# Performance work log

Measured on AMD Instinct MI355X. Metric: run time of the kernel, lower is better.

The kernel has to match this reference:

```python
import jax, jax.numpy as jnp
import numpy as np

B, N, C, H, P, DP = 2, 512, 384, 12, 4, 128
CH = C // H
SCALE = CH ** -0.5
EPS = 1e-5


def setup_inputs() -> dict:
    key = jax.random.key(0)
    ks = jax.random.split(key, 16)
    w = lambda k, i, o: jax.random.normal(k, (i, o), jnp.float32) * 0.02
    inp = {
        'single': jax.random.normal(ks[0], (B, N, C), jnp.float32),
        'pair': jax.random.normal(ks[1], (B, N, N, DP), jnp.float32),
        'rot': jax.random.normal(ks[2], (B, N, 3, 3), jnp.float32),
        'trans': jax.random.normal(ks[3], (B, N, 3), jnp.float32),
        'mask': jnp.ones((B, N), jnp.float32),
        'Wq': w(ks[4], C, C), 'bq': jnp.zeros((C,)),
        'Wk': w(ks[5], C, C), 'bk': jnp.zeros((C,)),
        'Wv': w(ks[6], C, C), 'bv': jnp.zeros((C,)),
        'Wpb': w(ks[7], DP, H), 'bpb': jnp.zeros((H,)),
        'Wqp': w(ks[8], C, H * P * 3), 'bqp': jnp.zeros((H * P * 3,)),
        'Wkp': w(ks[9], C, H * P * 3), 'bkp': jnp.zeros((H * P * 3,)),
        'Wvp': w(ks[10], C, H * P * 3), 'bvp': jnp.zeros((H * P * 3,)),
        'Wo': w(ks[11], C, C), 'bo': jnp.zeros((C,)),
        'Wpo': w(ks[12], H * P * 3, C), 'bpo': jnp.zeros((C,)),
        'ln_g': jnp.ones((C,)), 'ln_b': jnp.zeros((C,)),
    }
    return inp


def _to_global(pts, rot, trans):
    # pts: [B,N,H,P,3], rot: [B,N,3,3], trans: [B,N,3]
    return jnp.einsum('bnhpd,bnde->bnhpe', pts, rot) + trans[:, :, None, None, :]


def reference(single, pair, rot, trans, mask,
              Wq, bq, Wk, bk, Wv, bv, Wpb, bpb,
              Wqp, bqp, Wkp, bkp, Wvp, bvp,
              Wo, bo, Wpo, bpo, ln_g, ln_b):
    q = (single @ Wq + bq).reshape(B, N, H, CH)
    k = (single @ Wk + bk).reshape(B, N, H, CH)
    v = (single @ Wv + bv).reshape(B, N, H, CH)
    pair_bias = jnp.transpose(pair @ Wpb + bpb, (0, 3, 1, 2))  # [B,H,N,N]

    q_pts = (single @ Wqp + bqp).reshape(B, N, H, P, 3)
    k_pts = (single @ Wkp + bkp).reshape(B, N, H, P, 3)
    qg = _to_global(q_pts, rot, trans)
    kg = _to_global(k_pts, rot, trans)

    q2 = jnp.sum(qg * qg, axis=(3, 4))  # [B,N,H]
    k2 = jnp.sum(kg * kg, axis=(3, 4))
    qk = jnp.einsum('bnhpd,bmhpd->bhnm', qg, kg)
    q2h = jnp.transpose(q2, (0, 2, 1))  # [B,H,N]
    k2h = jnp.transpose(k2, (0, 2, 1))
    point_logits = -0.5 * (q2h[..., :, None] + k2h[..., None, :] - 2.0 * qk) * SCALE

    scalar_logits = jnp.einsum('bnhc,bmhc->bhnm', q, k) * SCALE
    logits = scalar_logits + pair_bias + point_logits

    mask2d = mask[:, None, :, None] * mask[:, None, None, :]  # [B,1,N,N]
    logits = jnp.where(mask2d == 0, -1e9, logits)
    attn = jax.nn.softmax(logits, axis=-1)

    weighted_scalar = jnp.einsum('bhnm,bmhc->bnhc', attn, v).reshape(B, N, C)

    v_pts = (single @ Wvp + bvp).reshape(B, N, H, P, 3)
    vg = _to_global(v_pts, rot, trans)
    weighted_points = jnp.einsum('bhnm,bmhpd->bnhpd', attn, vg).reshape(B, N, H * P * 3)

    point_proj = weighted_points @ Wpo + bpo
    out = (weighted_scalar + point_proj) @ Wo + bo

    x = single + out
    mu = jnp.mean(x, axis=-1, keepdims=True)
    var = jnp.mean((x - mu) ** 2, axis=-1, keepdims=True)
    return (x - mu) * jax.lax.rsqrt(var + EPS) * ln_g + ln_b
```

## Files before the change

### kernel.cpp

```cpp
#include <hip/hip_runtime.h>
#include <hip/hip_bf16.h>

#define Bb   2
#define Nn   512
#define Cc   384
#define Hh   12
#define BN   1024
#define NC1  1584
#define CT1  99
#define SCALE 0.17677669529663687f

typedef __attribute__((ext_vector_type(8))) short short8;
typedef __attribute__((ext_vector_type(4))) float f32x4;

__device__ __forceinline__ unsigned short f2bf(float f){
  union { float f; unsigned u; } v; v.f = f;
  unsigned u = v.u;
  unsigned r = u + 0x7fffu + ((u >> 16) & 1u);
  return (unsigned short)(r >> 16);
}
__device__ __forceinline__ float bf_lo(unsigned u){ union{unsigned u; float f;} v; v.u = u << 16; return v.f; }
__device__ __forceinline__ float bf_hi(unsigned u){ union{unsigned u; float f;} v; v.u = u & 0xffff0000u; return v.f; }
__device__ __forceinline__ unsigned pack2(float a, float b){
  return (unsigned)f2bf(a) | ((unsigned)f2bf(b) << 16);
}

__device__ __forceinline__ void bias_job(const float* __restrict__ pair,
    const float* __restrict__ Wpb, const float* __restrict__ bpb,
    unsigned short* __restrict__ biasf, int jid, int tid)
{
  int l = tid & 63, w = tid >> 6;
  long m0 = (long)jid * 64 + w * 16;
  long m = m0 + (l & 15);
  int kb = (l >> 4) << 3;
  int col = l & 15;
  short8 bf[4];
#pragma unroll
  for (int t = 0; t < 4; ++t){
#pragma unroll
    for (int j = 0; j < 8; ++j){
      int k = t * 32 + kb + j;
      float v = (col < 12) ? Wpb[k * 12 + col] : 0.f;
      bf[t][j] = (short)f2bf(v);
    }
  }
  const float* pr = pair + m * 128 + kb;
  f32x4 acc = {0,0,0,0};
#pragma unroll
  for (int t = 0; t < 4; ++t){
    float4 x0 = *(const float4*)(pr + t * 32);
    float4 x1 = *(const float4*)(pr + t * 32 + 4);
    short8 a;
    a[0] = (short)f2bf(x0.x); a[1] = (short)f2bf(x0.y);
    a[2] = (short)f2bf(x0.z); a[3] = (short)f2bf(x0.w);
    a[4] = (short)f2bf(x1.x); a[5] = (short)f2bf(x1.y);
    a[6] = (short)f2bf(x1.z); a[7] = (short)f2bf(x1.w);
    acc = __builtin_amdgcn_mfma_f32_16x16x32_bf16(a, bf[t], acc, 0, 0, 0);
  }
  int h = col;
  if (h < 12){
    long mr = m0 + ((l >> 4) << 2);
    int b  = (int)(mr >> 18);
    int i  = (int)((mr >> 9) & 511);
    int j  = (int)(mr & 511);
    int jt = j >> 5, f = (j >> 4) & 1, g2 = (j >> 2) & 3;
    int qt = i >> 4, q = i & 15;
    float bb = bpb[h];
    long e16 = (((((long)((b * 12 + h) * 16 + jt) * 32 + qt) * 2 + f) * 64) + (g2 * 16 + q)) * 4;
    uint2 wv; wv.x = pack2(acc[0] + bb, acc[1] + bb); wv.y = pack2(acc[2] + bb, acc[3] + bb);
    *(uint2*)(biasf + e16) = wv;
  }
}

__global__ __launch_bounds__(256) void k1_prep_bias(
    const float* __restrict__ single,
    const float* __restrict__ Wq, const float* __restrict__ Wk, const float* __restrict__ Wv,
    const float* __restrict__ Wqp, const float* __restrict__ Wkp, const float* __restrict__ Wvp,
    const float* __restrict__ bq, const float* __restrict__ bk, const float* __restrict__ bv,
    const float* __restrict__ bqp, const float* __restrict__ bkp, const float* __restrict__ bvp,
    const float* __restrict__ Wpo, const float* __restrict__ Wo,
    const float* __restrict__ pair, const float* __restrict__ Wpb, const float* __restrict__ bpb,
    unsigned short* __restrict__ sbf, unsigned short* __restrict__ wcat, float* __restrict__ bcat,
    unsigned short* __restrict__ wpof, unsigned short* __restrict__ wof,
    unsigned short* __restrict__ wppad, unsigned short* __restrict__ biasf)
{
  int bid = blockIdx.x, tid = threadIdx.x;
  if (bid >= 256){ bias_job(pair, Wpb, bpb, biasf, bid - 256, tid); return; }

  const int n0 = BN * Cc;
  const int n1 = 12 * CT1 * 512;
  const int n4 = NC1;
  const int n5 = 61440;
  const int n6 = 147456;
  const int n7 = BN * 16;
  const int total = n0 + n1 + n4 + n5 + n6 + n7;
  for (int i = bid * 256 + tid; i < total; i += 256 * 256){
    int e = i;
    if (e < n0){ sbf[e] = f2bf(single[e]); continue; }
    e -= n0;
    if (e < n1){
      int j8 = e & 7, l = (e >> 3) & 63, ctt = e >> 9;
      int ct = ctt % CT1, t = ctt / CT1;
      int k = t * 32 + ((l >> 4) << 3) + j8;
      int col = (ct << 4) + (l & 15);
      float v;
      if (col < 1152){
        const float* W = (col < 384) ? Wq : (col < 768 ? Wk : Wv);
        v = W[k * 384 + (col % 384)];
      } else {
        int c2 = col - 1152;
        const float* W = (c2 < 144) ? Wqp : (c2 < 288 ? Wkp : Wvp);
        v = W[k * 144 + (c2 % 144)];
      }
      wcat[e] = f2bf(v); continue;
    }
    e -= n1;
    if (e < n4){
      int col = e; float v;
      if (col < 1152){
        const float* bb = (col < 384) ? bq : (col < 768 ? bk : bv);
        v = bb[col % 384];
      } else {
        int c2 = col - 1152;
        const float* bb = (c2 < 144) ? bqp : (c2 < 288 ? bkp : bvp);
        v = bb[c2 % 144];
      }
      bcat[col] = v; continue;
    }
    e -= n4;
    if (e < n5){
      int j8 = e & 7, l = (e >> 3) & 63, ctt = e >> 9;
      int ct = ctt % 24, t = ctt / 24;
      int k = t * 32 + ((l >> 4) << 3) + j8;
      int col = (ct << 4) + (l & 15);
      wpof[e] = (k < 144) ? f2bf(Wpo[k * 384 + col]) : (unsigned short)0;
      continue;
    }
    e -= n5;
    if (e < n6){
      int j8 = e & 7, l = (e >> 3) & 63, ctt = e >> 9;
      int ct = ctt % 24, t = ctt / 24;
      int k = t * 32 + ((l >> 4) << 3) + j8;
      int col = (ct << 4) + (l & 15);
      wof[e] = f2bf(Wo[k * 384 + col]);
      continue;
    }
    e -= n6;
    { int row = e >> 4, c = e & 15; wppad[row * 160 + 144 + c] = 0; }
  }
}

__global__ __launch_bounds__(256) void k2_proj_bias(
    const unsigned short* __restrict__ sbf, const unsigned short* __restrict__ wcat,
    const float* __restrict__ bcat, float* __restrict__ proj,
    const float* __restrict__ pair, const float* __restrict__ Wpb, const float* __restrict__ bpb,
    unsigned short* __restrict__ biasf)
{
  int bid = blockIdx.x, tid = threadIdx.x;
  if (bid >= 528){ bias_job(pair, Wpb, bpb, biasf, 1024 + (bid - 528), tid); return; }

  int l = tid & 63, w = tid >> 6;
  int bx = bid & 15, by = bid >> 4;
  int m0 = bx * 64 + w * 16;
  const unsigned short* Ap = sbf + (long)(m0 + (l & 15)) * Cc + ((l >> 4) << 3);
  int ct0 = by * 3;
  f32x4 acc0 = {0,0,0,0}, acc1 = {0,0,0,0}, acc2 = {0,0,0,0};
  for (int t = 0; t < 12; ++t){
    short8 a = *(const short8*)(Ap + t * 32);
    const unsigned short* wp_ = wcat + ((long)(t * CT1 + ct0) * 64 + l) * 8;
    short8 b0 = *(const short8*)(wp_);
    short8 b1 = *(const short8*)(wp_ + 512);
    short8 b2 = *(const short8*)(wp_ + 1024);
    acc0 = __builtin_amdgcn_mfma_f32_16x16x32_bf16(a, b0, acc0, 0, 0, 0);
    acc1 = __builtin_amdgcn_mfma_f32_16x16x32_bf16(a, b1, acc1, 0, 0, 0);
    acc2 = __builtin_amdgcn_mfma_f32_16x16x32_bf16(a, b2, acc2, 0, 0, 0);
  }
  int rbase = m0 + ((l >> 4) << 2);
  int cb = by * 48 + (l & 15);
#pragma unroll
  for (int c = 0; c < 3; ++c){
    f32x4 ac = (c == 0) ? acc0 : (c == 1 ? acc1 : acc2);
    int col = cb + c * 16;
    float bb = bcat[col];
#pragma unroll
    for (int r = 0; r < 4; ++r)
      proj[(long)(rbase + r) * NC1 + col] = ac[r] + bb;
  }
}

__global__ __launch_bounds__(256) void k3_pack_bias(
    const float* __restrict__ proj, const float* __restrict__ rot,
    const float* __restrict__ trans, const float* __restrict__ mask,
    unsigned short* __restrict__ qf, unsigned short* __restrict__ kf,
    unsigned short* __restrict__ vf, float* __restrict__ q2h, float* __restrict__ k2h,
    const float* __restrict__ pair, const float* __restrict__ Wpb, const float* __restrict__ bpb,
    unsigned short* __restrict__ biasf)
{
  __shared__ float smemf[5792];
  int bid = blockIdx.x, tid = threadIdx.x;
  if (bid >= 384){ bias_job(pair, Wpb, bpb, biasf, 4096 + (bid - 384), tid); return; }

  float* scal = smemf;
  float* praw = scal + 3072;
  float* pg   = praw + 1152;
  float* rots = pg + 1152;
  float* trs  = rots + 288;
  float* msk  = trs + 96;

  int jid = bid;
  int b = jid / 192, rem = jid % 192;
  int h = rem >> 4, rt = rem & 15;
  int j0 = rt * 32;
  int bn0 = b * 512 + j0;
  int bh = b * 12 + h;

  for (int idx = tid; idx < 3072; idx += 256){
    int a = idx >> 10, row = (idx >> 5) & 31, c = idx & 31;
    scal[idx] = proj[(long)(bn0 + row) * NC1 + a * 384 + h * 32 + c];
  }
  for (int idx = tid; idx < 1152; idx += 256){
    int a = idx / 384, rr = idx % 384, row = rr / 12, pe = rr % 12;
    praw[idx] = proj[(long)(bn0 + row) * NC1 + 1152 + a * 144 + h * 12 + pe];
  }
  for (int idx = tid; idx < 288; idx += 256) rots[idx] = rot[(long)bn0 * 9 + idx];
  for (int idx = tid; idx < 96; idx += 256)  trs[idx] = trans[(long)bn0 * 3 + idx];
  for (int idx = tid; idx < 32; idx += 256)  msk[idx] = mask[bn0 + idx];
  __syncthreads();

  for (int idx = tid; idx < 1152; idx += 256){
    int a = idx / 384, rr = idx % 384, row = rr / 12, pe = rr % 12;
    int p = pe / 3, ee = pe % 3;
    pg[idx] = praw[a * 384 + row * 12 + p * 3] * rots[row * 9 + ee]
            + praw[a * 384 + row * 12 + p * 3 + 1] * rots[row * 9 + 3 + ee]
            + praw[a * 384 + row * 12 + p * 3 + 2] * rots[row * 9 + 6 + ee] + trs[row * 3 + ee];
  }
  __syncthreads();

  for (int idx = tid; idx < 64; idx += 256){
    int a = idx >> 5, row = idx & 31;
    float s2 = 0.f;
#pragma unroll
    for (int pe = 0; pe < 12; ++pe){ float g = pg[a * 384 + row * 12 + pe]; s2 += g * g; }
    float mv = msk[row];
    float rres = -0.5f * SCALE * s2 + (mv != 0.f ? 0.f : -2e9f);
    (a ? k2h : q2h)[(long)bh * 512 + j0 + row] = rres;
  }

  for (int idx = tid; idx < 2048; idx += 256){
    int a = idx >> 10, r = idx & 1023;
    int jjp = r & 3, l = (r >> 2) & 63, ks = (r >> 8) & 1, sub = r >> 9;
    int row = sub * 16 + (l & 15);
    int kk = ks * 32 + ((l >> 4) << 3) + jjp * 2;
    int k1 = kk + 1;
    float v0 = (kk < 32) ? scal[a * 1024 + row * 32 + kk] : (kk < 44 ? pg[a * 384 + row * 12 + kk - 32] : 0.f);
    float v1 = (k1 < 32) ? scal[a * 1024 + row * 32 + k1] : (k1 < 44 ? pg[a * 384 + row * 12 + k1 - 32] : 0.f);
    if (a == 0){ v0 *= SCALE; v1 *= SCALE; }
    unsigned* dst = (unsigned*)(a ? kf : qf);
    dst[((((long)bh * 32 + rt * 2 + sub) * 2 + ks) * 64 + l) * 4 + jjp] = pack2(v0, v1);
  }

  for (int idx = tid; idx < 768; idx += 256){
    int jjp = idx & 3, l = (idx >> 2) & 63, cf = idx >> 8;
    int c = cf * 16 + (l & 15);
    int j = ((l >> 4) << 3) + jjp * 2;
    float v0 = (c < 32) ? scal[2048 + j * 32 + c]       : (c < 44 ? pg[768 + j * 12 + (c - 32)]       : 0.f);
    float v1 = (c < 32) ? scal[2048 + (j + 1) * 32 + c] : (c < 44 ? pg[768 + (j + 1) * 12 + (c - 32)] : 0.f);
    ((unsigned*)vf)[(((long)bh * 16 + rt) * 3 + cf) * 256 + l * 4 + jjp] = pack2(v0, v1);
  }
}

__global__ __launch_bounds__(256) void attn2_kernel(
    const unsigned short* __restrict__ qf, const unsigned short* __restrict__ kf,
    const unsigned short* __restrict__ vf, const unsigned short* __restrict__ biasf,
    const float* __restrict__ q2h, const float* __restrict__ k2h,
    float* __restrict__ wsout, unsigned short* __restrict__ wpout)
{
  __shared__ unsigned short pls[4][16][40];
  __shared__ float oW[4][3][64][4];
  __shared__ float mW[4][16], lsW[4][16];
  __shared__ float fW[4][16], linvS[16];

  int l = threadIdx.x & 63, w = threadIdx.x >> 6;
  int qt = blockIdx.x, h = blockIdx.y, b = blockIdx.z;
  int bh = b * 12 + h;
  int g = l >> 4, q_ = l & 15;

  const short8* qp = (const short8*)(qf + (((long)(bh * 32 + qt) * 2) * 64 + l) * 8);
  short8 qA = qp[0], qB = qp[64];
  float cq = q2h[(long)bh * 512 + qt * 16 + q_];

  float m = -1e30f, ls = 0.f;
  f32x4 o0 = {0,0,0,0}, o1 = {0,0,0,0}, o2 = {0,0,0,0};
  const f32x4 z4 = {0,0,0,0};

#pragma unroll
  for (int ji = 0; ji < 4; ++ji){
    int jt = w * 4 + ji;
    const short8* kp = (const short8*)(kf + (((long)(bh * 32 + jt * 2) * 2) * 64 + l) * 8);
    short8 k00 = kp[0], k01 = kp[64], k10 = kp[128], k11 = kp[192];
    f32x4 s0 = __builtin_amdgcn_mfma_f32_16x16x32_bf16(k00, qA, z4, 0, 0, 0);
    s0 = __builtin_amdgcn_mfma_f32_16x16x32_bf16(k01, qB, s0, 0, 0, 0);
    f32x4 s1 = __builtin_amdgcn_mfma_f32_16x16x32_bf16(k10, qA, z4, 0, 0, 0);
    s1 = __builtin_amdgcn_mfma_f32_16x16x32_bf16(k11, qB, s1, 0, 0, 0);

    const uint2* bp = (const uint2*)(biasf + ((((long)(bh * 16 + jt) * 32 + qt) * 2) * 64) * 4);
    uint2 bb0 = bp[l], bb1 = bp[64 + l];
    const float4* k2p = (const float4*)(k2h + (long)bh * 512 + jt * 32);
    float4 ck0 = k2p[g], ck1 = k2p[4 + g];

    s0[0] += bf_lo(bb0.x) + cq + ck0.x;
    s0[1] += bf_hi(bb0.x) + cq + ck0.y;
    s0[2] += bf_lo(bb0.y) + cq + ck0.z;
    s0[3] += bf_hi(bb0.y) + cq + ck0.w;
    s1[0] += bf_lo(bb1.x) + cq + ck1.x;
    s1[1] += bf_hi(bb1.x) + cq + ck1.y;
    s1[2] += bf_lo(bb1.y) + cq + ck1.z;
    s1[3] += bf_hi(bb1.y) + cq + ck1.w;

    float tm = fmaxf(fmaxf(fmaxf(s0[0], s0[1]), fmaxf(s0[2], s0[3])),
                     fmaxf(fmaxf(s1[0], s1[1]), fmaxf(s1[2], s1[3])));
    tm = fmaxf(tm, __shfl_xor(tm, 16));
    tm = fmaxf(tm, __shfl_xor(tm, 32));
    float mn = fmaxf(m, tm);
    float alpha = __expf(m - mn);
    f32x4 p0, p1;
    float ts = 0.f;
#pragma unroll
    for (int r = 0; r < 4; ++r){ p0[r] = __expf(s0[r] - mn); ts += p0[r]; }
#pragma unroll
    for (int r = 0; r < 4; ++r){ p1[r] = __expf(s1[r] - mn); ts += p1[r]; }
    ts += __shfl_xor(ts, 16);
    ts += __shfl_xor(ts, 32);
    ls = ls * alpha + ts; m = mn;

    f32x4 av;
#pragma unroll
    for (int r = 0; r < 4; ++r) av[r] = __shfl(alpha, g * 4 + r);
#pragma unroll
    for (int r = 0; r < 4; ++r){ o0[r] *= av[r]; o1[r] *= av[r]; o2[r] *= av[r]; }

    uint2 w0; w0.x = pack2(p0[0], p0[1]); w0.y = pack2(p0[2], p0[3]);
    uint2 w1; w1.x = pack2(p1[0], p1[1]); w1.y = pack2(p1[2], p1[3]);
    *(uint2*)&pls[w][q_][g * 4]      = w0;
    *(uint2*)&pls[w][q_][16 + g * 4] = w1;
    short8 pa = *(const short8*)&pls[w][q_][g * 8];

    const short8* vp = (const short8*)(vf + (((long)(bh * 16 + jt) * 3) * 64 + l) * 8);
    short8 v0 = vp[0], v1 = vp[64], v2 = vp[128];
    o0 = __builtin_amdgcn_mfma_f32_16x16x32_bf16(pa, v0, o0, 0, 0, 0);
    o1 = __builtin_amdgcn_mfma_f32_16x16x32_bf16(pa, v1, o1, 0, 0, 0);
    o2 = __builtin_amdgcn_mfma_f32_16x16x32_bf16(pa, v2, o2, 0, 0, 0);
  }

  if (g == 0){ mW[w][q_] = m; lsW[w][q_] = ls; }
  *(f32x4*)&oW[w][0][l][0] = o0;
  *(f32x4*)&oW[w][1][l][0] = o1;
  *(f32x4*)&oW[w][2][l][0] = o2;
  __syncthreads();

  if (w == 0){
    float M = fmaxf(fmaxf(mW[0][q_], mW[1][q_]), fmaxf(mW[2][q_], mW[3][q_]));
    float f = __expf(mW[g][q_] - M);
    fW[g][q_] = f;
    float lf = lsW[g][q_] * f;
    lf += __shfl_xor(lf, 16);
    lf += __shfl_xor(lf, 32);
    if (g == 0) linvS[q_] = 1.f / lf;
  }
  __syncthreads();

  if (w < 3){
    float fr[4][4], li[4];
#pragma unroll
    for (int r = 0; r < 4; ++r){
      int q = g * 4 + r;
      li[r] = linvS[q];
#pragma unroll
      for (int vw = 0; vw < 4; ++vw) fr[vw][r] = fW[vw][q];
    }
    f32x4 sum = {0,0,0,0};
#pragma unroll
    for (int vw = 0; vw < 4; ++vw){
      f32x4 ov = *(const f32x4*)&oW[vw][w][l][0];
#pragma unroll
      for (int r = 0; r < 4; ++r) sum[r] += ov[r] * fr[vw][r];
    }
#pragma unroll
    for (int r = 0; r < 4; ++r){
      long bn = (long)b * 512 + qt * 16 + g * 4 + r;
      float val = sum[r] * li[r];
      if (w == 0)      wsout[bn * 384 + h * 32 + q_] = val;
      else if (w == 1) wsout[bn * 384 + h * 32 + 16 + q_] = val;
      else if (q_ < 12) wpout[bn * 160 + h * 12 + q_] = f2bf(val);
    }
  }
}

__global__ __launch_bounds__(256) void tail_kernel(
    const unsigned short* __restrict__ wpbuf, const unsigned short* __restrict__ wpof,
    const float* __restrict__ bpo, const float* __restrict__ wso,
    const unsigned short* __restrict__ wof, const float* __restrict__ bo,
    const float* __restrict__ single, const float* __restrict__ ln_g,
    const float* __restrict__ ln_b, float* __restrict__ out)
{
  __shared__ unsigned short t1s[16][392];
  __shared__ float redS[4][16], redQ[4][16];
  int l = threadIdx.x & 63, w = threadIdx.x >> 6;
  int m0 = blockIdx.x * 16;
  int rb = (l >> 4) << 2;
  int arow = m0 + (l & 15);

  {
    short8 awp[5];
    const unsigned short* Ap = wpbuf + (long)arow * 160 + ((l >> 4) << 3);
#pragma unroll
    for (int t = 0; t < 5; ++t) awp[t] = *(const short8*)(Ap + t * 32);
#pragma unroll
    for (int c6 = 0; c6 < 6; ++c6){
      int ct = w * 6 + c6;
      f32x4 acc = {0,0,0,0};
#pragma unroll
      for (int t = 0; t < 5; ++t){
        short8 bfr = *(const short8*)(wpof + ((long)(t * 24 + ct) * 64 + l) * 8);
        acc = __builtin_amdgcn_mfma_f32_16x16x32_bf16(awp[t], bfr, acc, 0, 0, 0);
      }
      int col = ct * 16 + (l & 15);
      float bb = bpo[col];
#pragma unroll
      for (int r = 0; r < 4; ++r){
        float v = acc[r] + bb + wso[(long)(m0 + rb + r) * 384 + col];
        t1s[rb + r][col] = f2bf(v);
      }
    }
  }
  __syncthreads();

  short8 a2[12];
  {
    int lr = l & 15;
#pragma unroll
    for (int t = 0; t < 12; ++t)
      a2[t] = *(const short8*)&t1s[lr][t * 32 + ((l >> 4) << 3)];
  }
  f32x4 xa[6];
  float s1[4] = {0,0,0,0}, s2[4] = {0,0,0,0};
#pragma unroll
  for (int c6 = 0; c6 < 6; ++c6){
    int ct = w * 6 + c6;
    f32x4 acc = {0,0,0,0};
#pragma unroll
    for (int t = 0; t < 12; ++t){
      short8 bfr = *(const short8*)(wof + ((long)(t * 24 + ct) * 64 + l) * 8);
      acc = __builtin_amdgcn_mfma_f32_16x16x32_bf16(a2[t], bfr, acc, 0, 0, 0);
    }
    int col = ct * 16 + (l & 15);
    float bb = bo[col];
#pragma unroll
    for (int r = 0; r < 4; ++r){
      float v = acc[r] + bb + single[(long)(m0 + rb + r) * 384 + col];
      acc[r] = v; s1[r] += v; s2[r] += v * v;
    }
    xa[c6] = acc;
  }
#pragma unroll
  for (int off = 1; off < 16; off <<= 1){
#pragma unroll
    for (int r = 0; r < 4; ++r){
      s1[r] += __shfl_xor(s1[r], off);
      s2[r] += __shfl_xor(s2[r], off);
    }
  }
  if ((l & 15) == 0){
#pragma unroll
    for (int r = 0; r < 4; ++r){ redS[w][rb + r] = s1[r]; redQ[w][rb + r] = s2[r]; }
  }
  __syncthreads();
  float mu[4], inv[4];
#pragma unroll
  for (int r = 0; r < 4; ++r){
    float ts = redS[0][rb + r] + redS[1][rb + r] + redS[2][rb + r] + redS[3][rb + r];
    float tq = redQ[0][rb + r] + redQ[1][rb + r] + redQ[2][rb + r] + redQ[3][rb + r];
    mu[r] = ts * (1.f / 384.f);
    float var = tq * (1.f / 384.f) - mu[r] * mu[r];
    inv[r] = rsqrtf(var + 1e-5f);
  }
#pragma unroll
  for (int c6 = 0; c6 < 6; ++c6){
    int ct = w * 6 + c6;
    int col = ct * 16 + (l & 15);
    float g = ln_g[col], bt = ln_b[col];
#pragma unroll
    for (int r = 0; r < 4; ++r)
      out[(long)(m0 + rb + r) * 384 + col] = (xa[c6][r] - mu[r]) * inv[r] * g + bt;
  }
}

extern "C" void kernel_launch(void* const* d_in, const int* in_sizes, int n_in,
                              void* d_out, int out_size, void* d_ws, size_t ws_size,
                              hipStream_t stream)
{
  const float* single = (const float*)d_in[0];
  const float* pair   = (const float*)d_in[1];
  const float* rot    = (const float*)d_in[2];
  const float* trans  = (const float*)d_in[3];
  const float* mask   = (const float*)d_in[4];
  const float* Wq  = (const float*)d_in[5];  const float* bq  = (const float*)d_in[6];
  const float* Wk  = (const float*)d_in[7];  const float* bk  = (const float*)d_in[8];
  const float* Wv  = (const float*)d_in[9];  const float* bv  = (const float*)d_in[10];
  const float* Wpb = (const float*)d_in[11]; const float* bpb = (const float*)d_in[12];
  const float* Wqp = (const float*)d_in[13]; const float* bqp = (const float*)d_in[14];
  const float* Wkp = (const float*)d_in[15]; const float* bkp = (const float*)d_in[16];
  const float* Wvp = (const float*)d_in[17]; const float* bvp = (const float*)d_in[18];
  const float* Wo  = (const float*)d_in[19]; const float* bo  = (const float*)d_in[20];
  const float* Wpo = (const float*)d_in[21]; const float* bpo = (const float*)d_in[22];
  const float* ln_g = (const float*)d_in[23]; const float* ln_b = (const float*)d_in[24];

  char* wsb = (char*)d_ws;
  size_t off = 0;
  auto alloc = [&](size_t bytes) -> void* {
    void* p = wsb + off; off += (bytes + 255) & ~(size_t)255; return p;
  };
  unsigned short* sbf  = (unsigned short*)alloc((size_t)BN * Cc * 2);
  unsigned short* wcat = (unsigned short*)alloc((size_t)12 * CT1 * 512 * 2);
  unsigned short* wpof = (unsigned short*)alloc((size_t)5 * 24 * 512 * 2);
  unsigned short* wof  = (unsigned short*)alloc((size_t)12 * 24 * 512 * 2);
  float* bcat  = (float*)alloc(NC1 * 4);
  float* proj  = (float*)alloc((size_t)BN * NC1 * 4);
  unsigned short* biasf = (unsigned short*)alloc((size_t)Bb * Hh * Nn * Nn * 2);
  unsigned short* qfragb = (unsigned short*)alloc((size_t)786432 * 2);
  unsigned short* kfragb = (unsigned short*)alloc((size_t)786432 * 2);
  unsigned short* vfragb = (unsigned short*)alloc((size_t)589824 * 2);
  float* q2hb  = (float*)alloc((size_t)12288 * 4);
  float* k2hb  = (float*)alloc((size_t)12288 * 4);
  float* wso   = (float*)alloc((size_t)BN * 384 * 4);
  unsigned short* wpbuf = (unsigned short*)alloc((size_t)BN * 160 * 2);
  if (off > ws_size) return;

  k1_prep_bias<<<256 + 1024, 256, 0, stream>>>(
      single, Wq, Wk, Wv, Wqp, Wkp, Wvp, bq, bk, bv, bqp, bkp, bvp, Wpo, Wo,
      pair, Wpb, bpb, sbf, wcat, bcat, wpof, wof, wpbuf, biasf);
  k2_proj_bias<<<528 + 3072, 256, 0, stream>>>(
      sbf, wcat, bcat, proj, pair, Wpb, bpb, biasf);
  k3_pack_bias<<<384 + 4096, 256, 0, stream>>>(
      proj, rot, trans, mask, qfragb, kfragb, vfragb, q2hb, k2hb,
      pair, Wpb, bpb, biasf);
  attn2_kernel<<<dim3(32, 12, 2), 256, 0, stream>>>(qfragb, kfragb, vfragb, biasf,
                                                    q2hb, k2hb, wso, wpbuf);
  tail_kernel<<<64, 256, 0, stream>>>(wpbuf, wpof, bpo, wso, wof, bo,
                                      single, ln_g, ln_b, (float*)d_out);
}
```

Measured before the change: 106.2 us.

## Overlap pair-bias computation with per-batch attention and tail across fused kernels

Splits the attention kernel by batch so that batch 0 attention runs in the same launch as the last part of the pair-bias projection (batch 1), and batch 1 attention runs alongside the tail for batch 0. The bias work in k3 is halved and the remainder moves into k4, which lets the bias, attention and tail stages run concurrently instead of serially. This adds a kernel launch and depends on the bias job indices and batch boundaries being split correctly, so that batch 0's bias is complete before k4 and batch 1's bias is complete before k5.

```diff
diff --git a/kernel.cpp b/kernel.cpp
--- a/kernel.cpp
+++ b/kernel.cpp
@@ -69,6 +69,238 @@
     long e16 = (((((long)((b * 12 + h) * 16 + jt) * 32 + qt) * 2 + f) * 64) + (g2 * 16 + q)) * 4;
     uint2 wv; wv.x = pack2(acc[0] + bb, acc[1] + bb); wv.y = pack2(acc[2] + bb, acc[3] + bb);
     *(uint2*)(biasf + e16) = wv;
+  }
+}
+
+__device__ __forceinline__ void attn_job(
+    const unsigned short* __restrict__ qf, const unsigned short* __restrict__ kf,
+    const unsigned short* __restrict__ vf, const unsigned short* __restrict__ biasf,
+    const float* __restrict__ q2h, const float* __restrict__ k2h,
+    float* __restrict__ wsout, unsigned short* __restrict__ wpout,
+    int b, int jid, int tid, unsigned char* smem)
+{
+  unsigned short* pls = (unsigned short*)smem;
+  float* oW   = (float*)(smem + 5120);
+  float* mW   = (float*)(smem + 17408);
+  float* lsW  = (float*)(smem + 17664);
+  float* fW   = (float*)(smem + 17920);
+  float* linvS= (float*)(smem + 18176);
+
+  int l = tid & 63, w = tid >> 6;
+  int qt = jid & 31, h = jid >> 5;
+  int bh = b * 12 + h;
+  int g = l >> 4, q_ = l & 15;
+
+  const short8* qp = (const short8*)(qf + (((long)(bh * 32 + qt) * 2) * 64 + l) * 8);
+  short8 qA = qp[0], qB = qp[64];
+  float cq = q2h[(long)bh * 512 + qt * 16 + q_];
+
+  float m = -1e30f, ls = 0.f;
+  f32x4 o0 = {0,0,0,0}, o1 = {0,0,0,0}, o2 = {0,0,0,0};
+  const f32x4 z4 = {0,0,0,0};
+
+#pragma unroll
+  for (int ji = 0; ji < 4; ++ji){
+    int jt = w * 4 + ji;
+    const short8* kp = (const short8*)(kf + (((long)(bh * 32 + jt * 2) * 2) * 64 + l) * 8);
+    short8 k00 = kp[0], k01 = kp[64], k10 = kp[128], k11 = kp[192];
+    f32x4 s0 = __builtin_amdgcn_mfma_f32_16x16x32_bf16(k00, qA, z4, 0, 0, 0);
+    s0 = __builtin_amdgcn_mfma_f32_16x16x32_bf16(k01, qB, s0, 0, 0, 0);
+    f32x4 s1 = __builtin_amdgcn_mfma_f32_16x16x32_bf16(k10, qA, z4, 0, 0, 0);
+    s1 = __builtin_amdgcn_mfma_f32_16x16x32_bf16(k11, qB, s1, 0, 0, 0);
+
+    const uint2* bp = (const uint2*)(biasf + ((((long)(bh * 16 + jt) * 32 + qt) * 2) * 64) * 4);
+    uint2 bb0 = bp[l], bb1 = bp[64 + l];
+    const float4* k2p = (const float4*)(k2h + (long)bh * 512 + jt * 32);
+    float4 ck0 = k2p[g], ck1 = k2p[4 + g];
+
+    s0[0] += bf_lo(bb0.x) + cq + ck0.x;
+    s0[1] += bf_hi(bb0.x) + cq + ck0.y;
+    s0[2] += bf_lo(bb0.y) + cq + ck0.z;
+    s0[3] += bf_hi(bb0.y) + cq + ck0.w;
+    s1[0] += bf_lo(bb1.x) + cq + ck1.x;
+    s1[1] += bf_hi(bb1.x) + cq + ck1.y;
+    s1[2] += bf_lo(bb1.y) + cq + ck1.z;
+    s1[3] += bf_hi(bb1.y) + cq + ck1.w;
+
+    float tm = fmaxf(fmaxf(fmaxf(s0[0], s0[1]), fmaxf(s0[2], s0[3])),
+                     fmaxf(fmaxf(s1[0], s1[1]), fmaxf(s1[2], s1[3])));
+    tm = fmaxf(tm, __shfl_xor(tm, 16));
+    tm = fmaxf(tm, __shfl_xor(tm, 32));
+    float mn = fmaxf(m, tm);
+    float alpha = __expf(m - mn);
+    f32x4 p0, p1;
+    float ts = 0.f;
+#pragma unroll
+    for (int r = 0; r < 4; ++r){ p0[r] = __expf(s0[r] - mn); ts += p0[r]; }
+#pragma unroll
+    for (int r = 0; r < 4; ++r){ p1[r] = __expf(s1[r] - mn); ts += p1[r]; }
+    ts += __shfl_xor(ts, 16);
+    ts += __shfl_xor(ts, 32);
+    ls = ls * alpha + ts; m = mn;
+
+    f32x4 av;
+#pragma unroll
+    for (int r = 0; r < 4; ++r) av[r] = __shfl(alpha, g * 4 + r);
+#pragma unroll
+    for (int r = 0; r < 4; ++r){ o0[r] *= av[r]; o1[r] *= av[r]; o2[r] *= av[r]; }
+
+    uint2 w0; w0.x = pack2(p0[0], p0[1]); w0.y = pack2(p0[2], p0[3]);
+    uint2 w1; w1.x = pack2(p1[0], p1[1]); w1.y = pack2(p1[2], p1[3]);
+    *(uint2*)&pls[(w * 16 + q_) * 40 + g * 4]      = w0;
+    *(uint2*)&pls[(w * 16 + q_) * 40 + 16 + g * 4] = w1;
+    short8 pa = *(const short8*)&pls[(w * 16 + q_) * 40 + g * 8];
+
+    const short8* vp = (const short8*)(vf + (((long)(bh * 16 + jt) * 3) * 64 + l) * 8);
+    short8 v0 = vp[0], v1 = vp[64], v2 = vp[128];
+    o0 = __builtin_amdgcn_mfma_f32_16x16x32_bf16(pa, v0, o0, 0, 0, 0);
+    o1 = __builtin_amdgcn_mfma_f32_16x16x32_bf16(pa, v1, o1, 0, 0, 0);
+    o2 = __builtin_amdgcn_mfma_f32_16x16x32_bf16(pa, v2, o2, 0, 0, 0);
+  }
+
+  if (g == 0){ mW[w * 16 + q_] = m; lsW[w * 16 + q_] = ls; }
+  *(f32x4*)&oW[((w * 3 + 0) * 64 + l) * 4] = o0;
+  *(f32x4*)&oW[((w * 3 + 1) * 64 + l) * 4] = o1;
+  *(f32x4*)&oW[((w * 3 + 2) * 64 + l) * 4] = o2;
+  __syncthreads();
+
+  if (w == 0){
+    float M = fmaxf(fmaxf(mW[q_], mW[16 + q_]), fmaxf(mW[32 + q_], mW[48 + q_]));
+    float f = __expf(mW[g * 16 + q_] - M);
+    fW[g * 16 + q_] = f;
+    float lf = lsW[g * 16 + q_] * f;
+    lf += __shfl_xor(lf, 16);
+    lf += __shfl_xor(lf, 32);
+    if (g == 0) linvS[q_] = 1.f / lf;
+  }
+  __syncthreads();
+
+  if (w < 3){
+    float fr[4][4], li[4];
+#pragma unroll
+    for (int r = 0; r < 4; ++r){
+      int q = g * 4 + r;
+      li[r] = linvS[q];
+#pragma unroll
+      for (int vw = 0; vw < 4; ++vw) fr[vw][r] = fW[vw * 16 + q];
+    }
+    f32x4 sum = {0,0,0,0};
+#pragma unroll
+    for (int vw = 0; vw < 4; ++vw){
+      f32x4 ov = *(const f32x4*)&oW[((vw * 3 + w) * 64 + l) * 4];
+#pragma unroll
+      for (int r = 0; r < 4; ++r) sum[r] += ov[r] * fr[vw][r];
+    }
+#pragma unroll
+    for (int r = 0; r < 4; ++r){
+      long bn = (long)b * 512 + qt * 16 + g * 4 + r;
+      float val = sum[r] * li[r];
+      if (w == 0)      wsout[bn * 384 + h * 32 + q_] = val;
+      else if (w == 1) wsout[bn * 384 + h * 32 + 16 + q_] = val;
+      else if (q_ < 12) wpout[bn * 160 + h * 12 + q_] = f2bf(val);
+    }
+  }
+}
+
+__device__ __forceinline__ void tail_job(
+    const unsigned short* __restrict__ wpbuf, const unsigned short* __restrict__ wpof,
+    const float* __restrict__ bpo, const float* __restrict__ wso,
+    const unsigned short* __restrict__ wof, const float* __restrict__ bo,
+    const float* __restrict__ single, const float* __restrict__ ln_g,
+    const float* __restrict__ ln_b, float* __restrict__ out,
+    int jid, int tid, unsigned char* smem)
+{
+  unsigned short* t1s = (unsigned short*)smem;
+  float* redS = (float*)(smem + 12544);
+  float* redQ = (float*)(smem + 12800);
+
+  int l = tid & 63, w = tid >> 6;
+  int m0 = jid * 16;
+  int rb = (l >> 4) << 2;
+  int arow = m0 + (l & 15);
+
+  {
+    short8 awp[5];
+    const unsigned short* Ap = wpbuf + (long)arow * 160 + ((l >> 4) << 3);
+#pragma unroll
+    for (int t = 0; t < 5; ++t) awp[t] = *(const short8*)(Ap + t * 32);
+#pragma unroll
+    for (int c6 = 0; c6 < 6; ++c6){
+      int ct = w * 6 + c6;
+      f32x4 acc = {0,0,0,0};
+#pragma unroll
+      for (int t = 0; t < 5; ++t){
+        short8 bfr = *(const short8*)(wpof + ((long)(t * 24 + ct) * 64 + l) * 8);
+        acc = __builtin_amdgcn_mfma_f32_16x16x32_bf16(awp[t], bfr, acc, 0, 0, 0);
+      }
+      int col = ct * 16 + (l & 15);
+      float bb = bpo[col];
+#pragma unroll
+      for (int r = 0; r < 4; ++r){
+        float v = acc[r] + bb + wso[(long)(m0 + rb + r) * 384 + col];
+        t1s[(rb + r) * 392 + col] = f2bf(v);
+      }
+    }
+  }
+  __syncthreads();
+
+  short8 a2[12];
+  {
+    int lr = l & 15;
+#pragma unroll
+    for (int t = 0; t < 12; ++t)
+      a2[t] = *(const short8*)&t1s[lr * 392 + t * 32 + ((l >> 4) << 3)];
+  }
+  f32x4 xa[6];
+  float s1[4] = {0,0,0,0}, s2[4] = {0,0,0,0};
+#pragma unroll
+  for (int c6 = 0; c6 < 6; ++c6){
+    int ct = w * 6 + c6;
+    f32x4 acc = {0,0,0,0};
+#pragma unroll
+    for (int t = 0; t < 12; ++t){
+      short8 bfr = *(const short8*)(wof + ((long)(t * 24 + ct) * 64 + l) * 8);
+      acc = __builtin_amdgcn_mfma_f32_16x16x32_bf16(a2[t], bfr, acc, 0, 0, 0);
+    }
+    int col = ct * 16 + (l & 15);
+    float bb = bo[col];
+#pragma unroll
+    for (int r = 0; r < 4; ++r){
+      float v = acc[r] + bb + single[(long)(m0 + rb + r) * 384 + col];
+      acc[r] = v; s1[r] += v; s2[r] += v * v;
+    }
+    xa[c6] = acc;
+  }
+#pragma unroll
+  for (int off = 1; off < 16; off <<= 1){
+#pragma unroll
+    for (int r = 0; r < 4; ++r){
+      s1[r] += __shfl_xor(s1[r], off);
+      s2[r] += __shfl_xor(s2[r], off);
+    }
+  }
+  if ((l & 15) == 0){
+#pragma unroll
+    for (int r = 0; r < 4; ++r){ redS[w * 16 + rb + r] = s1[r]; redQ[w * 16 + rb + r] = s2[r]; }
+  }
+  __syncthreads();
+  float mu[4], inv[4];
+#pragma unroll
+  for (int r = 0; r < 4; ++r){
+    float ts = redS[rb + r] + redS[16 + rb + r] + redS[32 + rb + r] + redS[48 + rb + r];
+    float tq = redQ[rb + r] + redQ[16 + rb + r] + redQ[32 + rb + r] + redQ[48 + rb + r];
+    mu[r] = ts * (1.f / 384.f);
+    float var = tq * (1.f / 384.f) - mu[r] * mu[r];
+    inv[r] = rsqrtf(var + 1e-5f);
+  }
+#pragma unroll
+  for (int c6 = 0; c6 < 6; ++c6){
+    int ct = w * 6 + c6;
+    int col = ct * 16 + (l & 15);
+    float g = ln_g[col], bt = ln_b[col];
+#pragma unroll
+    for (int r = 0; r < 4; ++r)
+      out[(long)(m0 + rb + r) * 384 + col] = (xa[c6][r] - mu[r]) * inv[r] * g + bt;
   }
 }
 
@@ -269,230 +501,50 @@
   }
 }
 
-__global__ __launch_bounds__(256) void attn2_kernel(
+__global__ __launch_bounds__(256) void k4_attn_bias(
     const unsigned short* __restrict__ qf, const unsigned short* __restrict__ kf,
     const unsigned short* __restrict__ vf, const unsigned short* __restrict__ biasf,
     const float* __restrict__ q2h, const float* __restrict__ k2h,
-    float* __restrict__ wsout, unsigned short* __restrict__ wpout)
-{
-  __shared__ unsigned short pls[4][16][40];
-  __shared__ float oW[4][3][64][4];
-  __shared__ float mW[4][16], lsW[4][16];
-  __shared__ float fW[4][16], linvS[16];
-
-  int l = threadIdx.x & 63, w = threadIdx.x >> 6;
-  int qt = blockIdx.x, h = blockIdx.y, b = blockIdx.z;
-  int bh = b * 12 + h;
-  int g = l >> 4, q_ = l & 15;
-
-  const short8* qp = (const short8*)(qf + (((long)(bh * 32 + qt) * 2) * 64 + l) * 8);
-  short8 qA = qp[0], qB = qp[64];
-  float cq = q2h[(long)bh * 512 + qt * 16 + q_];
-
-  float m = -1e30f, ls = 0.f;
-  f32x4 o0 = {0,0,0,0}, o1 = {0,0,0,0}, o2 = {0,0,0,0};
-  const f32x4 z4 = {0,0,0,0};
-
-#pragma unroll
-  for (int ji = 0; ji < 4; ++ji){
-    int jt = w * 4 + ji;
-    const short8* kp = (const short8*)(kf + (((long)(bh * 32 + jt * 2) * 2) * 64 + l) * 8);
-    short8 k00 = kp[0], k01 = kp[64], k10 = kp[128], k11 = kp[192];
-    f32x4 s0 = __builtin_amdgcn_mfma_f32_16x16x32_bf16(k00, qA, z4, 0, 0, 0);
-    s0 = __builtin_amdgcn_mfma_f32_16x16x32_bf16(k01, qB, s0, 0, 0, 0);
-    f32x4 s1 = __builtin_amdgcn_mfma_f32_16x16x32_bf16(k10, qA, z4, 0, 0, 0);
-    s1 = __builtin_amdgcn_mfma_f32_16x16x32_bf16(k11, qB, s1, 0, 0, 0);
-
-    const uint2* bp = (const uint2*)(biasf + ((((long)(bh * 16 + jt) * 32 + qt) * 2) * 64) * 4);
-    uint2 bb0 = bp[l], bb1 = bp[64 + l];
-    const float4* k2p = (const float4*)(k2h + (long)bh * 512 + jt * 32);
-    float4 ck0 = k2p[g], ck1 = k2p[4 + g];
-
-    s0[0] += bf_lo(bb0.x) + cq + ck0.x;
-    s0[1] += bf_hi(bb0.x) + cq + ck0.y;
-    s0[2] += bf_lo(bb0.y) + cq + ck0.z;
-    s0[3] += bf_hi(bb0.y) + cq + ck0.w;
-    s1[0] += bf_lo(bb1.x) + cq + ck1.x;
-    s1[1] += bf_hi(bb1.x) + cq + ck1.y;
-    s1[2] += bf_lo(bb1.y) + cq + ck1.z;
-    s1[3] += bf_hi(bb1.y) + cq + ck1.w;
-
-    float tm = fmaxf(fmaxf(fmaxf(s0[0], s0[1]), fmaxf(s0[2], s0[3])),
-                     fmaxf(fmaxf(s1[0], s1[1]), fmaxf(s1[2], s1[3])));
-    tm = fmaxf(tm, __shfl_xor(tm, 16));
-    tm = fmaxf(tm, __shfl_xor(tm, 32));
-    float mn = fmaxf(m, tm);
-    float alpha = __expf(m - mn);
-    f32x4 p0, p1;
-    float ts = 0.f;
-#pragma unroll
-    for (int r = 0; r < 4; ++r){ p0[r] = __expf(s0[r] - mn); ts += p0[r]; }
-#pragma unroll
-    for (int r = 0; r < 4; ++r){ p1[r] = __expf(s1[r] - mn); ts += p1[r]; }
-    ts += __shfl_xor(ts, 16);
-    ts += __shfl_xor(ts, 32);
-    ls = ls * alpha + ts; m = mn;
-
-    f32x4 av;
-#pragma unroll
-    for (int r = 0; r < 4; ++r) av[r] = __shfl(alpha, g * 4 + r);
-#pragma unroll
-    for (int r = 0; r < 4; ++r){ o0[r] *= av[r]; o1[r] *= av[r]; o2[r] *= av[r]; }
-
-    uint2 w0; w0.x = pack2(p0[0], p0[1]); w0.y = pack2(p0[2], p0[3]);
-    uint2 w1; w1.x = pack2(p1[0], p1[1]); w1.y = pack2(p1[2], p1[3]);
-    *(uint2*)&pls[w][q_][g * 4]      = w0;
-    *(uint2*)&pls[w][q_][16 + g * 4] = w1;
-    short8 pa = *(const short8*)&pls[w][q_][g * 8];
-
-    const short8* vp = (const short8*)(vf + (((long)(bh * 16 + jt) * 3) * 64 + l) * 8);
-    short8 v0 = vp[0], v1 = vp[64], v2 = vp[128];
-    o0 = __builtin_amdgcn_mfma_f32_16x16x32_bf16(pa, v0, o0, 0, 0, 0);
-    o1 = __builtin_amdgcn_mfma_f32_16x16x32_bf16(pa, v1, o1, 0, 0, 0);
-    o2 = __builtin_amdgcn_mfma_f32_16x16x32_bf16(pa, v2, o2, 0, 0, 0);
-  }
-
-  if (g == 0){ mW[w][q_] = m; lsW[w][q_] = ls; }
-  *(f32x4*)&oW[w][0][l][0] = o0;
-  *(f32x4*)&oW[w][1][l][0] = o1;
-  *(f32x4*)&oW[w][2][l][0] = o2;
-  __syncthreads();
-
-  if (w == 0){
-    float M = fmaxf(fmaxf(mW[0][q_], mW[1][q_]), fmaxf(mW[2][q_], mW[3][q_]));
-    float f = __expf(mW[g][q_] - M);
-    fW[g][q_] = f;
-    float lf = lsW[g][q_] * f;
-    lf += __shfl_xor(lf, 16);
-    lf += __shfl_xor(lf, 32);
-    if (g == 0) linvS[q_] = 1.f / lf;
-  }
-  __syncthreads();
-
-  if (w < 3){
-    float fr[4][4], li[4];
-#pragma unroll
-    for (int r = 0; r < 4; ++r){
-      int q = g * 4 + r;
-      li[r] = linvS[q];
-#pragma unroll
-      for (int vw = 0; vw < 4; ++vw) fr[vw][r] = fW[vw][q];
-    }
-    f32x4 sum = {0,0,0,0};
-#pragma unroll
-    for (int vw = 0; vw < 4; ++vw){
-      f32x4 ov = *(const f32x4*)&oW[vw][w][l][0];
-#pragma unroll
-      for (int r = 0; r < 4; ++r) sum[r] += ov[r] * fr[vw][r];
-    }
-#pragma unroll
-    for (int r = 0; r < 4; ++r){
-      long bn = (long)b * 512 + qt * 16 + g * 4 + r;
-      float val = sum[r] * li[r];
-      if (w == 0)      wsout[bn * 384 + h * 32 + q_] = val;
-      else if (w == 1) wsout[bn * 384 + h * 32 + 16 + q_] = val;
-      else if (q_ < 12) wpout[bn * 160 + h * 12 + q_] = f2bf(val);
-    }
-  }
-}
-
-__global__ __launch_bounds__(256) void tail_kernel(
+    float* __restrict__ wso, unsigned short* __restrict__ wpbuf,
+    const float* __restrict__ pair, const float* __restrict__ Wpb, const float* __restrict__ bpb,
+    unsigned short* __restrict__ biasf_w)
+{
+  __shared__ __align__(16) unsigned char smem[18304];
+  int bid = blockIdx.x, tid = threadIdx.x;
+  if (bid >= 384){ bias_job(pair, Wpb, bpb, biasf_w, 6144 + (bid - 384), tid); return; }
+  attn_job(qf, kf, vf, biasf, q2h, k2h, wso, wpbuf, 0, bid, tid, smem);
+}
+
+__global__ __launch_bounds__(256) void k5_attn_tail(
+    const unsigned short* __restrict__ qf, const unsigned short* __restrict__ kf,
+    const unsigned short* __restrict__ vf, const unsigned short* __restrict__ biasf,
+    const float* __restrict__ q2h, const float* __restrict__ k2h,
+    float* __restrict__ wso, unsigned short* __restrict__ wpbuf,
+    const unsigned short* __restrict__ wpof, const float* __restrict__ bpo,
+    const unsigned short* __restrict__ wof, const float* __restrict__ bo,
+    const float* __restrict__ single, const float* __restrict__ ln_g,
+    const float* __restrict__ ln_b, float* __restrict__ out)
+{
+  __shared__ __align__(16) unsigned char smem[18304];
+  int bid = blockIdx.x, tid = threadIdx.x;
+  if (bid < 384){
+    attn_job(qf, kf, vf, biasf, q2h, k2h, wso, wpbuf, 1, bid, tid, smem);
+  } else {
+    tail_job(wpbuf, wpof, bpo, wso, wof, bo, single, ln_g, ln_b, out,
+             bid - 384, tid, smem);
+  }
+}
+
+__global__ __launch_bounds__(256) void k6_tail(
     const unsigned short* __restrict__ wpbuf, const unsigned short* __restrict__ wpof,
     const float* __restrict__ bpo, const float* __restrict__ wso,
     const unsigned short* __restrict__ wof, const float* __restrict__ bo,
     const float* __restrict__ single, const float* __restrict__ ln_g,
     const float* __restrict__ ln_b, float* __restrict__ out)
 {
-  __shared__ unsigned short t1s[16][392];
-  __shared__ float redS[4][16], redQ[4][16];
-  int l = threadIdx.x & 63, w = threadIdx.x >> 6;
-  int m0 = blockIdx.x * 16;
-  int rb = (l >> 4) << 2;
-  int arow = m0 + (l & 15);
-
-  {
-    short8 awp[5];
-    const unsigned short* Ap = wpbuf + (long)arow * 160 + ((l >> 4) << 3);
-#pragma unroll
-    for (int t = 0; t < 5; ++t) awp[t] = *(const short8*)(Ap + t * 32);
-#pragma unroll
-    for (int c6 = 0; c6 < 6; ++c6){
-      int ct = w * 6 + c6;
-      f32x4 acc = {0,0,0,0};
-#pragma unroll
-      for (int t = 0; t < 5; ++t){
-        short8 bfr = *(const short8*)(wpof + ((long)(t * 24 + ct) * 64 + l) * 8);
-        acc = __builtin_amdgcn_mfma_f32_16x16x32_bf16(awp[t], bfr, acc, 0, 0, 0);
-      }
-      int col = ct * 16 + (l & 15);
-      float bb = bpo[col];
-#pragma unroll
-      for (int r = 0; r < 4; ++r){
-        float v = acc[r] + bb + wso[(long)(m0 + rb + r) * 384 + col];
-        t1s[rb + r][col] = f2bf(v);
-      }
-    }
-  }
-  __syncthreads();
-
-  short8 a2[12];
-  {
-    int lr = l & 15;
-#pragma unroll
-    for (int t = 0; t < 12; ++t)
-      a2[t] = *(const short8*)&t1s[lr][t * 32 + ((l >> 4) << 3)];
-  }
-  f32x4 xa[6];
-  float s1[4] = {0,0,0,0}, s2[4] = {0,0,0,0};
-#pragma unroll
-  for (int c6 = 0; c6 < 6; ++c6){
-    int ct = w * 6 + c6;
-    f32x4 acc = {0,0,0,0};
-#pragma unroll
-    for (int t = 0; t < 12; ++t){
-      short8 bfr = *(const short8*)(wof + ((long)(t * 24 + ct) * 64 + l) * 8);
-      acc = __builtin_amdgcn_mfma_f32_16x16x32_bf16(a2[t], bfr, acc, 0, 0, 0);
-    }
-    int col = ct * 16 + (l & 15);
-    float bb = bo[col];
-#pragma unroll
-    for (int r = 0; r < 4; ++r){
-      float v = acc[r] + bb + single[(long)(m0 + rb + r) * 384 + col];
-      acc[r] = v; s1[r] += v; s2[r] += v * v;
-    }
-    xa[c6] = acc;
-  }
-#pragma unroll
-  for (int off = 1; off < 16; off <<= 1){
-#pragma unroll
-    for (int r = 0; r < 4; ++r){
-      s1[r] += __shfl_xor(s1[r], off);
-      s2[r] += __shfl_xor(s2[r], off);
-    }
-  }
-  if ((l & 15) == 0){
-#pragma unroll
-    for (int r = 0; r < 4; ++r){ redS[w][rb + r] = s1[r]; redQ[w][rb + r] = s2[r]; }
-  }
-  __syncthreads();
-  float mu[4], inv[4];
-#pragma unroll
-  for (int r = 0; r < 4; ++r){
-    float ts = redS[0][rb + r] + redS[1][rb + r] + redS[2][rb + r] + redS[3][rb + r];
-    float tq = redQ[0][rb + r] + redQ[1][rb + r] + redQ[2][rb + r] + redQ[3][rb + r];
-    mu[r] = ts * (1.f / 384.f);
-    float var = tq * (1.f / 384.f) - mu[r] * mu[r];
-    inv[r] = rsqrtf(var + 1e-5f);
-  }
-#pragma unroll
-  for (int c6 = 0; c6 < 6; ++c6){
-    int ct = w * 6 + c6;
-    int col = ct * 16 + (l & 15);
-    float g = ln_g[col], bt = ln_b[col];
-#pragma unroll
-    for (int r = 0; r < 4; ++r)
-      out[(long)(m0 + rb + r) * 384 + col] = (xa[c6][r] - mu[r]) * inv[r] * g + bt;
-  }
+  __shared__ __align__(16) unsigned char smem[13056];
+  tail_job(wpbuf, wpof, bpo, wso, wof, bo, single, ln_g, ln_b, out,
+           32 + blockIdx.x, threadIdx.x, smem);
 }
 
 extern "C" void kernel_launch(void* const* d_in, const int* in_sizes, int n_in,
@@ -541,11 +593,15 @@
       pair, Wpb, bpb, sbf, wcat, bcat, wpof, wof, wpbuf, biasf);
   k2_proj_bias<<<528 + 3072, 256, 0, stream>>>(
       sbf, wcat, bcat, proj, pair, Wpb, bpb, biasf);
-  k3_pack_bias<<<384 + 4096, 256, 0, stream>>>(
+  k3_pack_bias<<<384 + 2048, 256, 0, stream>>>(
       proj, rot, trans, mask, qfragb, kfragb, vfragb, q2hb, k2hb,
       pair, Wpb, bpb, biasf);
-  attn2_kernel<<<dim3(32, 12, 2), 256, 0, stream>>>(qfragb, kfragb, vfragb, biasf,
-                                                    q2hb, k2hb, wso, wpbuf);
-  tail_kernel<<<64, 256, 0, stream>>>(wpbuf, wpof, bpo, wso, wof, bo,
-                                      single, ln_g, ln_b, (float*)d_out);
-}
+  k4_attn_bias<<<384 + 2048, 256, 0, stream>>>(
+      qfragb, kfragb, vfragb, biasf, q2hb, k2hb, wso, wpbuf,
+      pair, Wpb, bpb, biasf);
+  k5_attn_tail<<<384 + 32, 256, 0, stream>>>(
+      qfragb, kfragb, vfragb, biasf, q2hb, k2hb, wso, wpbuf,
+      wpof, bpo, wof, bo, single, ln_g, ln_b, (float*)d_out);
+  k6_tail<<<32, 256, 0, stream>>>(
+      wpbuf, wpof, bpo, wso, wof, bo, single, ln_g, ln_b, (float*)d_out);
+}
```

Measured after the change: 109.9 us. 3.5% more time.

## Stage pair-bias tiles through LDS for coalesced fragment-layout stores

Applied to the files above, without the earlier changes.

The pair-bias projection job now gives each block a 16x32 (i,j) tile across all heads. It runs 8 MFMA sub-tiles per block, writes the results into shared memory, then writes them out to the attention fragment layout as contiguous runs, where before each lane did a scattered 8-byte store. This cuts the number of bias blocks by a factor of 8 and is meant to coalesce the biasf writes. The cost is added LDS use and a __syncthreads in blocks that also host other work in the same kernels. Launch sizes are adjusted to match.

```diff
diff --git a/kernel.cpp b/kernel.cpp
--- a/kernel.cpp
+++ b/kernel.cpp
@@ -25,50 +25,62 @@
   return (unsigned)f2bf(a) | ((unsigned)f2bf(b) << 16);
 }
 
-__device__ __forceinline__ void bias_job(const float* __restrict__ pair,
+__device__ __forceinline__ void bias_job16(const float* __restrict__ pair,
     const float* __restrict__ Wpb, const float* __restrict__ bpb,
-    unsigned short* __restrict__ biasf, int jid, int tid)
+    unsigned short* __restrict__ biasf, int jd, int tid, unsigned short* lds)
 {
   int l = tid & 63, w = tid >> 6;
-  long m0 = (long)jid * 64 + w * 16;
-  long m = m0 + (l & 15);
+  int b = jd >> 9, r9 = jd & 511;
+  int it = r9 >> 4, jt = r9 & 15;
+  int i0 = it << 4, j0 = jt << 5;
   int kb = (l >> 4) << 3;
-  int col = l & 15;
+  int h = l & 15;
   short8 bf[4];
 #pragma unroll
   for (int t = 0; t < 4; ++t){
 #pragma unroll
     for (int j = 0; j < 8; ++j){
       int k = t * 32 + kb + j;
-      float v = (col < 12) ? Wpb[k * 12 + col] : 0.f;
+      float v = (h < 12) ? Wpb[k * 12 + h] : 0.f;
       bf[t][j] = (short)f2bf(v);
     }
   }
-  const float* pr = pair + m * 128 + kb;
-  f32x4 acc = {0,0,0,0};
-#pragma unroll
-  for (int t = 0; t < 4; ++t){
-    float4 x0 = *(const float4*)(pr + t * 32);
-    float4 x1 = *(const float4*)(pr + t * 32 + 4);
-    short8 a;
-    a[0] = (short)f2bf(x0.x); a[1] = (short)f2bf(x0.y);
-    a[2] = (short)f2bf(x0.z); a[3] = (short)f2bf(x0.w);
-    a[4] = (short)f2bf(x1.x); a[5] = (short)f2bf(x1.y);
-    a[6] = (short)f2bf(x1.z); a[7] = (short)f2bf(x1.w);
-    acc = __builtin_amdgcn_mfma_f32_16x16x32_bf16(a, bf[t], acc, 0, 0, 0);
-  }
-  int h = col;
-  if (h < 12){
-    long mr = m0 + ((l >> 4) << 2);
-    int b  = (int)(mr >> 18);
-    int i  = (int)((mr >> 9) & 511);
-    int j  = (int)(mr & 511);
-    int jt = j >> 5, f = (j >> 4) & 1, g2 = (j >> 2) & 3;
-    int qt = i >> 4, q = i & 15;
-    float bb = bpb[h];
-    long e16 = (((((long)((b * 12 + h) * 16 + jt) * 32 + qt) * 2 + f) * 64) + (g2 * 16 + q)) * 4;
-    uint2 wv; wv.x = pack2(acc[0] + bb, acc[1] + bb); wv.y = pack2(acc[2] + bb, acc[3] + bb);
-    *(uint2*)(biasf + e16) = wv;
+  float bb = (h < 12) ? bpb[h] : 0.f;
+
+  for (int s = 0; s < 8; ++s){
+    int tile = s * 4 + w;
+    int iloc = tile >> 1, jh = tile & 1;
+    long m = ((long)(b * 512 + i0 + iloc)) * 512 + j0 + jh * 16 + (l & 15);
+    const float* pr = pair + m * 128 + kb;
+    f32x4 acc = {0,0,0,0};
+#pragma unroll
+    for (int t = 0; t < 4; ++t){
+      float4 x0 = *(const float4*)(pr + t * 32);
+      float4 x1 = *(const float4*)(pr + t * 32 + 4);
+      short8 a;
+      a[0] = (short)f2bf(x0.x); a[1] = (short)f2bf(x0.y);
+      a[2] = (short)f2bf(x0.z); a[3] = (short)f2bf(x0.w);
+      a[4] = (short)f2bf(x1.x); a[5] = (short)f2bf(x1.y);
+      a[6] = (short)f2bf(x1.z); a[7] = (short)f2bf(x1.w);
+      acc = __builtin_amdgcn_mfma_f32_16x16x32_bf16(a, bf[t], acc, 0, 0, 0);
+    }
+    if (h < 12){
+      int jloc = jh * 16 + ((l >> 4) << 2);
+      unsigned short* dst = lds + (h * 17 + iloc) * 36 + jloc;
+      uint2 wv; wv.x = pack2(acc[0] + bb, acc[1] + bb); wv.y = pack2(acc[2] + bb, acc[3] + bb);
+      *(uint2*)dst = wv;
+    }
+  }
+  __syncthreads();
+
+  for (int e = tid; e < 12 * 2 * 64; e += 256){
+    int run = e >> 6, idx = e & 63;
+    int h2 = run >> 1, f = run & 1;
+    int g2 = idx >> 4, q = idx & 15;
+    const unsigned short* src = lds + (h2 * 17 + q) * 36 + f * 16 + g2 * 4;
+    uint2 v = *(const uint2*)src;
+    long base = ((((long)(b * 12 + h2) * 16 + jt) * 32 + it) * 2 + f) * 64 + idx;
+    *(uint2*)(biasf + base * 4) = v;
   }
 }
 
@@ -84,8 +96,9 @@
     unsigned short* __restrict__ wpof, unsigned short* __restrict__ wof,
     unsigned short* __restrict__ wppad, unsigned short* __restrict__ biasf)
 {
+  __shared__ __align__(16) unsigned short blds[16 * 17 * 36];
   int bid = blockIdx.x, tid = threadIdx.x;
-  if (bid >= 256){ bias_job(pair, Wpb, bpb, biasf, bid - 256, tid); return; }
+  if (bid >= 256){ bias_job16(pair, Wpb, bpb, biasf, bid - 256, tid, blds); return; }
 
   const int n0 = BN * Cc;
   const int n1 = 12 * CT1 * 512;
@@ -156,8 +169,9 @@
     const float* __restrict__ pair, const float* __restrict__ Wpb, const float* __restrict__ bpb,
     unsigned short* __restrict__ biasf)
 {
+  __shared__ __align__(16) unsigned short blds[16 * 17 * 36];
   int bid = blockIdx.x, tid = threadIdx.x;
-  if (bid >= 528){ bias_job(pair, Wpb, bpb, biasf, 1024 + (bid - 528), tid); return; }
+  if (bid >= 528){ bias_job16(pair, Wpb, bpb, biasf, 192 + (bid - 528), tid, blds); return; }
 
   int l = tid & 63, w = tid >> 6;
   int bx = bid & 15, by = bid >> 4;
@@ -196,11 +210,14 @@
     const float* __restrict__ pair, const float* __restrict__ Wpb, const float* __restrict__ bpb,
     unsigned short* __restrict__ biasf)
 {
-  __shared__ float smemf[5792];
+  __shared__ __align__(16) unsigned char smem3[23168];
   int bid = blockIdx.x, tid = threadIdx.x;
-  if (bid >= 384){ bias_job(pair, Wpb, bpb, biasf, 4096 + (bid - 384), tid); return; }
-
-  float* scal = smemf;
+  if (bid >= 384){
+    bias_job16(pair, Wpb, bpb, biasf, 576 + (bid - 384), tid, (unsigned short*)smem3);
+    return;
+  }
+
+  float* scal = (float*)smem3;
   float* praw = scal + 3072;
   float* pg   = praw + 1152;
   float* rots = pg + 1152;
@@ -536,12 +553,12 @@
   unsigned short* wpbuf = (unsigned short*)alloc((size_t)BN * 160 * 2);
   if (off > ws_size) return;
 
-  k1_prep_bias<<<256 + 1024, 256, 0, stream>>>(
+  k1_prep_bias<<<256 + 192, 256, 0, stream>>>(
       single, Wq, Wk, Wv, Wqp, Wkp, Wvp, bq, bk, bv, bqp, bkp, bvp, Wpo, Wo,
       pair, Wpb, bpb, sbf, wcat, bcat, wpof, wof, wpbuf, biasf);
-  k2_proj_bias<<<528 + 3072, 256, 0, stream>>>(
+  k2_proj_bias<<<528 + 384, 256, 0, stream>>>(
       sbf, wcat, bcat, proj, pair, Wpb, bpb, biasf);
-  k3_pack_bias<<<384 + 4096, 256, 0, stream>>>(
+  k3_pack_bias<<<384 + 448, 256, 0, stream>>>(
       proj, rot, trans, mask, qfragb, kfragb, vfragb, q2hb, k2hb,
       pair, Wpb, bpb, biasf);
   attn2_kernel<<<dim3(32, 12, 2), 256, 0, stream>>>(qfragb, kfragb, vfragb, biasf,
```

Result: faster. 96.12 us (-9.5%).
